# Kernel optimization log

Measured on AMD Instinct MI355X. Metric: run time of the kernel, lower is better.

## Reference

```python
import jax, jax.numpy as jnp
import numpy as np
from math import sqrt

B, H, S, D = 4, 16, 2048, 64
NEG = -1000000000.0

def setup_inputs() -> dict:
    key = jax.random.key(0)
    kq, kk, kv, km = jax.random.split(key, 4)
    Q = jax.random.normal(kq, (B, H, S, D), dtype=jnp.float32)
    K = jax.random.normal(kk, (B, H, S, D), dtype=jnp.float32)
    V = jax.random.normal(kv, (B, H, S, D), dtype=jnp.float32)
    mask = jax.random.uniform(km, (B, 1, S, S)) < 0.1
    return {"Q": Q, "K": K, "V": V, "mask": mask}

def reference(Q, K, V, mask) -> jnp.ndarray:
    # scores: [B,H,S,S]
    scores = jnp.einsum('bhqd,bhkd->bhqk', Q, K)
    scores = jnp.where(mask, NEG, scores)
    attn = jax.nn.softmax(scores / sqrt(Q.shape[-1]), axis=-1)
    return jnp.einsum('bhqk,bhkd->bhqd', attn, V)
```

## Files before the change

kernel.cpp:

```cpp
#include <hip/hip_runtime.h>


#define SEQ 2048
#define DIM 64
#define NBH 64
#define LOG2E 1.44269504088896340736f
#define SCL (0.125f * LOG2E)
#define NEG_SCALED -1.25e8f

typedef short bf16x8 __attribute__((ext_vector_type(8)));
typedef float f32x4 __attribute__((ext_vector_type(4)));
typedef float f32x16 __attribute__((ext_vector_type(16)));

static __device__ __forceinline__ unsigned short f2bf(float f) {
    unsigned int u = __float_as_uint(f);
    u += 0x7fffu + ((u >> 16) & 1u);
    return (unsigned short)(u >> 16);
}

#define GLD16(gp, lp) __builtin_amdgcn_global_load_lds( \
    (const __attribute__((address_space(1))) unsigned int*)(gp), \
    (__attribute__((address_space(3))) unsigned int*)(lp), 16, 0, 0)

__global__ __launch_bounds__(256)
void prep_all_kernel(const float* __restrict__ K, const float* __restrict__ V,
                     const int* __restrict__ M,
                     unsigned short* __restrict__ Kb, unsigned short* __restrict__ Vt,
                     unsigned int* __restrict__ Mpt) {
    const int x = blockIdx.x;
    const int t = threadIdx.x;
    if (x < 4096) {
        size_t i0 = ((size_t)x * 256 + t) * 8;
        float4 a = *(const float4*)(K + i0);
        float4 b = *(const float4*)(K + i0 + 4);
        union { uint4 u; unsigned short s[8]; } w;
        w.s[0] = f2bf(a.x); w.s[1] = f2bf(a.y); w.s[2] = f2bf(a.z); w.s[3] = f2bf(a.w);
        w.s[4] = f2bf(b.x); w.s[5] = f2bf(b.y); w.s[6] = f2bf(b.z); w.s[7] = f2bf(b.w);
        *(uint4*)(Kb + i0) = w.u;
    } else if (x < 6144) {
        __shared__ __align__(16) unsigned short T[64 * 64];
        const int vb = x - 4096;
        const int bh = vb >> 5;
        const int k0 = (vb & 31) * 64;
        {
            const float* Vb = V + ((size_t)bh * SEQ + k0) * DIM;
            #pragma unroll
            for (int j = 0; j < 4; ++j) {
                const int fi = (j * 256 + t) * 4;
                const int kk = fi >> 6;
                const int d0 = fi & 63;
                float4 f = *(const float4*)(Vb + fi);
                const int u  = (kk & ~12) | ((kk & 4) << 1) | ((kk & 8) >> 1);
                const int cs = (d0 >> 4) ^ ((u >> 3) & 3);
                union { uint2 q; unsigned short s[4]; } w4;
                w4.s[0] = f2bf(f.x); w4.s[1] = f2bf(f.y);
                w4.s[2] = f2bf(f.z); w4.s[3] = f2bf(f.w);
                *(uint2*)&T[u * 64 + cs * 16 + (d0 & 15)] = w4.q;
            }
        }
        __syncthreads();
        {
            const int kc = t & 7;
            const int dp = t >> 3;
            const int ch = (dp >> 3) ^ (kc & 3);
            const unsigned int* T32 = (const unsigned int*)T;
            union { uint4 u; unsigned short s[8]; } o0, o1;
            #pragma unroll
            for (int i = 0; i < 8; ++i) {
                unsigned int v = T32[(8 * kc + i) * 32 + ch * 8 + (dp & 7)];
                o0.s[i] = (unsigned short)v;
                o1.s[i] = (unsigned short)(v >> 16);
            }
            unsigned short* op = Vt + ((size_t)bh * DIM + 2 * dp) * SEQ + k0 + 8 * kc;
            *(uint4*)op         = o0.u;
            *(uint4*)(op + SEQ) = o1.u;
        }
    } else {
        __shared__ unsigned int Wt[64][8];
        const int m  = x - 6144;
        const int b  = m >> 8;
        const int q0 = ((m >> 3) & 31) * 64;
        const int k0 = (m & 7) * 256;
        const int w  = t >> 6, l = t & 63;
        #pragma unroll 4
        for (int row = 0; row < 16; ++row) {
            const int q = q0 + w * 16 + row;
            int4 v4 = *(const int4*)(M + ((size_t)b * SEQ + q) * SEQ + k0 + l * 4);
            unsigned int nib = (unsigned int)(v4.x != 0) | ((unsigned int)(v4.y != 0) << 1)
                             | ((unsigned int)(v4.z != 0) << 2) | ((unsigned int)(v4.w != 0) << 3);
            unsigned int v = nib << (4 * (l & 7));
            v |= __shfl_xor(v, 1);
            v |= __shfl_xor(v, 2);
            v |= __shfl_xor(v, 4);
            if ((l & 7) == 0) Wt[w * 16 + row][l >> 3] = v;
        }
        __syncthreads();
        {
            const int q = t & 63, g0 = t >> 6;
            #pragma unroll
            for (int gg = 0; gg < 2; ++gg) {
                const int g = g0 + gg * 4;
                Mpt[((size_t)b * 64 + (k0 >> 5) + g) * SEQ + q0 + q] = Wt[q][g];
            }
        }
    }
}

__global__ __launch_bounds__(256, 4)
void attn_main_kernel(const float* __restrict__ Q,
                      const unsigned short* __restrict__ Kb,
                      const unsigned short* __restrict__ Vt,
                      const unsigned int* __restrict__ Mpt,
                      float* __restrict__ O)
{
    const int n    = blockIdx.y * gridDim.x + blockIdx.x;
    const int bh   = ((n & 7) << 3) | (n >> 7);
    const int q0   = ((n >> 3) & 15) * 128;
    const int b    = bh >> 4;
    const int tid  = threadIdx.x;
    const int wave = tid >> 6;
    const int lane = tid & 63;
    const int h    = lane >> 5;
    const int q32  = lane & 31;
    const int sh4  = 4 * h;

    __shared__ __align__(16) unsigned short Kt[2][32 * 64];
    __shared__ __align__(16) unsigned short Vs[2][64 * 32];

    const unsigned short* Kbh = Kb + (size_t)bh * SEQ * DIM;
    const unsigned short* Vbh = Vt + (size_t)bh * SEQ * DIM;

    bf16x8 qf[4];
    {
        const float* qp = Q + ((size_t)bh * SEQ + q0 + wave * 32 + q32) * DIM + h * 8;
        #pragma unroll
        for (int dc = 0; dc < 4; ++dc) {
            float4 xx = *(const float4*)(qp + dc * 16);
            float4 yy = *(const float4*)(qp + dc * 16 + 4);
            qf[dc][0] = (short)f2bf(xx.x * SCL); qf[dc][1] = (short)f2bf(xx.y * SCL);
            qf[dc][2] = (short)f2bf(xx.z * SCL); qf[dc][3] = (short)f2bf(xx.w * SCL);
            qf[dc][4] = (short)f2bf(yy.x * SCL); qf[dc][5] = (short)f2bf(yy.y * SCL);
            qf[dc][6] = (short)f2bf(yy.z * SCL); qf[dc][7] = (short)f2bf(yy.w * SCL);
        }
    }

    const int kkey  = wave * 8 + (lane >> 3);
    const int kclog = (lane & 7) ^ (lane >> 3);
    const unsigned short* kg = Kbh + (size_t)kkey * DIM + kclog * 8;
    const int vd    = wave * 16 + (lane >> 2);
    const int vclog = (lane & 3) ^ ((lane >> 3) & 3);
    const unsigned short* vg = Vbh + (size_t)vd * SEQ + vclog * 8;
    unsigned short* kl[2] = { &Kt[0][wave * 512], &Kt[1][wave * 512] };
    unsigned short* vl[2] = { &Vs[0][wave * 512], &Vs[1][wave * 512] };

    const unsigned int* mp = Mpt + (size_t)b * 64 * SEQ + (q0 + wave * 32 + q32);

    f32x16 acc[2];
    #pragma unroll
    for (int i = 0; i < 16; ++i) { acc[0][i] = 0.f; acc[1][i] = 0.f; }
    float ls0 = 0.f, ls1 = 0.f, ls2 = 0.f, ls3 = 0.f;

    GLD16(kg, kl[0]);
    GLD16(vg, vl[0]);
    unsigned int mw = mp[0];

    #pragma unroll 2
    for (int it = 0; it < SEQ / 32; ++it) {
        __syncthreads();

        unsigned int mw_n = 0;
        if (it + 1 < SEQ / 32) {
            const unsigned short* kgn = kg + (size_t)(it + 1) * 32 * DIM;
            const unsigned short* vgn = vg + (size_t)(it + 1) * 32;
            int nb = (it + 1) & 1;
            GLD16(kgn, kl[nb]);
            GLD16(vgn, vl[nb]);
            mw_n = mp[(it + 1) * SEQ];
        }

        const unsigned short* Ktb = Kt[it & 1];
        const unsigned short* Vsb = Vs[it & 1];

        const unsigned int mq = mw >> sh4;
        f32x16 sc;
        #pragma unroll
        for (int r = 0; r < 16; ++r) {
            const int s = (r & 3) + 8 * (r >> 2);
            sc[r] = __int_as_float(__builtin_amdgcn_sbfe(mq, s, 1) & 0xC2C80000u);
        }

        __builtin_amdgcn_s_setprio(1);
        #pragma unroll
        for (int dc = 0; dc < 4; ++dc) {
            const int pos = (dc * 2 + h) ^ (q32 & 7);
            bf16x8 kf = *(const bf16x8*)(Ktb + q32 * 64 + pos * 8);
            sc = __builtin_amdgcn_mfma_f32_32x32x16_bf16(kf, qf[dc], sc, 0, 0, 0);
        }
        __builtin_amdgcn_s_setprio(0);

        float pv[16];
        #pragma unroll
        for (int r = 0; r < 16; ++r) pv[r] = __builtin_amdgcn_exp2f(sc[r]);

        #pragma unroll
        for (int r = 0; r < 16; r += 4) {
            ls0 += pv[r + 0];
            ls1 += pv[r + 1];
            ls2 += pv[r + 2];
            ls3 += pv[r + 3];
        }

        unsigned int pk[8];
        #pragma unroll
        for (int m = 0; m < 8; ++m) {
            asm("v_cvt_pk_bf16_f32 %0, %1, %2"
                : "=v"(pk[m]) : "v"(pv[2 * m]), "v"(pv[2 * m + 1]));
        }

        __builtin_amdgcn_s_setprio(1);
        #pragma unroll
        for (int kk = 0; kk < 2; ++kk) {
            union { unsigned int u[4]; bf16x8 v; } fr;
            fr.u[0] = pk[4 * kk + 0];
            fr.u[1] = pk[4 * kk + 1];
            fr.u[2] = pk[4 * kk + 2];
            fr.u[3] = pk[4 * kk + 3];
            #pragma unroll
            for (int dh = 0; dh < 2; ++dh) {
                const int d   = dh * 32 + q32;
                const int pos = (kk * 2 + h) ^ ((q32 >> 1) & 3);
                bf16x8 vf = *(const bf16x8*)(Vsb + d * 32 + pos * 8);
                acc[dh] = __builtin_amdgcn_mfma_f32_32x32x16_bf16(vf, fr.v, acc[dh], 0, 0, 0);
            }
        }
        __builtin_amdgcn_s_setprio(0);

        mw = mw_n;
    }

    float lsum = (ls0 + ls1) + (ls2 + ls3);
    lsum += __shfl_xor(lsum, 32);
    const float inv = 1.f / lsum;
    float* orow = O + ((size_t)bh * SEQ + q0 + wave * 32 + q32) * DIM;
    #pragma unroll
    for (int dh = 0; dh < 2; ++dh) {
        #pragma unroll
        for (int r23 = 0; r23 < 4; ++r23) {
            float4 w;
            w.x = acc[dh][4 * r23 + 0] * inv;
            w.y = acc[dh][4 * r23 + 1] * inv;
            w.z = acc[dh][4 * r23 + 2] * inv;
            w.w = acc[dh][4 * r23 + 3] * inv;
            *(float4*)(orow + dh * 32 + r23 * 8 + h * 4) = w;
        }
    }
}

__global__ __launch_bounds__(256)
void attn_fallback_kernel(const float* __restrict__ Q,
                          const float* __restrict__ K,
                          const float* __restrict__ V,
                          const int* __restrict__ mask,
                          float* __restrict__ O)
{
    const int bh   = blockIdx.y;
    const int b    = bh >> 4;
    const int q0   = blockIdx.x * 64;
    const int tid  = threadIdx.x;
    const int wave = tid >> 6;
    const int lane = tid & 63;
    const int quad = lane >> 4;
    const int l16  = lane & 15;

    __shared__ __align__(16) unsigned short Klds[32][72];
    __shared__ __align__(16) unsigned short VT[64][40];
    __shared__ __align__(16) unsigned short Plds[4][16][40];

    const float* Qb = Q + (size_t)bh * SEQ * DIM;
    const float* Kb = K + (size_t)bh * SEQ * DIM;
    const float* Vb = V + (size_t)bh * SEQ * DIM;
    const int*   Mb = mask + (size_t)b * SEQ * SEQ;

    const int qrow_frag = q0 + wave * 16 + l16;
    bf16x8 qf0, qf1;
    {
        const float* qp = Qb + (size_t)qrow_frag * DIM + quad * 8;
        #pragma unroll
        for (int i = 0; i < 8; ++i) {
            qf0[i] = (short)f2bf(qp[i]);
            qf1[i] = (short)f2bf(qp[32 + i]);
        }
    }

    f32x4 acc[4];
    #pragma unroll
    for (int dg = 0; dg < 4; ++dg) acc[dg] = (f32x4){0.f, 0.f, 0.f, 0.f};
    float mrowv[4] = {-INFINITY, -INFINITY, -INFINITY, -INFINITY};
    float lrow[4] = {0.f, 0.f, 0.f, 0.f};

    const int skey = tid >> 3;
    const int sd0  = (tid & 7) * 8;
    const int vkey = tid & 31;
    const int vd0  = (tid >> 5) * 8;
    const int qrow_m = q0 + wave * 16 + quad * 4;

    for (int kb = 0; kb < SEQ; kb += 32) {
        __syncthreads();
        {
            const float* kp = Kb + (size_t)(kb + skey) * DIM + sd0;
            union { uint4 u4; unsigned short s[8]; } kw;
            #pragma unroll
            for (int i = 0; i < 8; ++i) kw.s[i] = f2bf(kp[i]);
            *(uint4*)&Klds[skey][sd0] = kw.u4;
        }
        {
            const float* vp = Vb + (size_t)(kb + vkey) * DIM + vd0;
            #pragma unroll
            for (int i = 0; i < 8; ++i) VT[vd0 + i][vkey] = f2bf(vp[i]);
        }
        __syncthreads();

        f32x4 scr[2];
        scr[0] = (f32x4){0.f, 0.f, 0.f, 0.f};
        scr[1] = (f32x4){0.f, 0.f, 0.f, 0.f};
        #pragma unroll
        for (int nt = 0; nt < 2; ++nt) {
            bf16x8 kf0 = *(const bf16x8*)&Klds[nt * 16 + l16][quad * 8];
            bf16x8 kf1 = *(const bf16x8*)&Klds[nt * 16 + l16][32 + quad * 8];
            scr[nt] = __builtin_amdgcn_mfma_f32_16x16x32_bf16(qf0, kf0, scr[nt], 0, 0, 0);
            scr[nt] = __builtin_amdgcn_mfma_f32_16x16x32_bf16(qf1, kf1, scr[nt], 0, 0, 0);
        }

        float x[2][4];
        #pragma unroll
        for (int nt = 0; nt < 2; ++nt)
            #pragma unroll
            for (int r = 0; r < 4; ++r) {
                int mv = Mb[(size_t)(qrow_m + r) * SEQ + kb + nt * 16 + l16];
                x[nt][r] = mv ? NEG_SCALED : scr[nt][r] * 0.125f;
            }

        float p[2][4];
        #pragma unroll
        for (int r = 0; r < 4; ++r) {
            float rm = fmaxf(x[0][r], x[1][r]);
            #pragma unroll
            for (int off = 1; off < 16; off <<= 1)
                rm = fmaxf(rm, __shfl_xor(rm, off, 16));
            float mn = fmaxf(mrowv[r], rm);
            float alpha = exp2f((mrowv[r] - mn) * LOG2E);
            mrowv[r] = mn;
            float p0 = exp2f((x[0][r] - mn) * LOG2E);
            float p1 = exp2f((x[1][r] - mn) * LOG2E);
            p[0][r] = p0; p[1][r] = p1;
            float rs = p0 + p1;
            #pragma unroll
            for (int off = 1; off < 16; off <<= 1)
                rs += __shfl_xor(rs, off, 16);
            lrow[r] = lrow[r] * alpha + rs;
            #pragma unroll
            for (int dg = 0; dg < 4; ++dg)
                acc[dg][r] *= alpha;
        }

        #pragma unroll
        for (int nt = 0; nt < 2; ++nt)
            #pragma unroll
            for (int r = 0; r < 4; ++r)
                Plds[wave][quad * 4 + r][nt * 16 + l16] = f2bf(p[nt][r]);

        bf16x8 pf = *(const bf16x8*)&Plds[wave][l16][quad * 8];

        #pragma unroll
        for (int dg = 0; dg < 4; ++dg) {
            bf16x8 vf = *(const bf16x8*)&VT[dg * 16 + l16][quad * 8];
            acc[dg] = __builtin_amdgcn_mfma_f32_16x16x32_bf16(pf, vf, acc[dg], 0, 0, 0);
        }
    }

    float* Ob = O + (size_t)bh * SEQ * DIM;
    #pragma unroll
    for (int r = 0; r < 4; ++r) {
        float inv = 1.f / lrow[r];
        #pragma unroll
        for (int dg = 0; dg < 4; ++dg)
            Ob[(size_t)(qrow_m + r) * DIM + dg * 16 + l16] = acc[dg][r] * inv;
    }
}

extern "C" void kernel_launch(void* const* d_in, const int* in_sizes, int n_in,
                              void* d_out, int out_size, void* d_ws, size_t ws_size,
                              hipStream_t stream) {
    const float* Q = (const float*)d_in[0];
    const float* K = (const float*)d_in[1];
    const float* V = (const float*)d_in[2];
    const int* mask = (const int*)d_in[3];
    float*        O = (float*)d_out;

    const size_t szK = (size_t)NBH * SEQ * DIM * 2;
    const size_t szV = (size_t)NBH * SEQ * DIM * 2;
    const size_t szM = (size_t)4 * SEQ * (SEQ / 32) * 4;
    const size_t need = szK + szV + szM;

    if (ws_size >= need) {
        unsigned short* Kb = (unsigned short*)d_ws;
        unsigned short* Vt = (unsigned short*)((char*)d_ws + szK);
        unsigned int*  Mpt = (unsigned int*)((char*)d_ws + szK + szV);

        prep_all_kernel<<<dim3(7168), 256, 0, stream>>>(K, V, mask, Kb, Vt, Mpt);
        attn_main_kernel<<<dim3(SEQ / 128, NBH), 256, 0, stream>>>(Q, Kb, Vt, Mpt, O);
    } else {
        attn_fallback_kernel<<<dim3(SEQ / 64, NBH), 256, 0, stream>>>(Q, K, V, mask, O);
    }
}
```

Baseline: 270.6 us.

## Process two 32-key tiles per barrier and reorder prep kernel blocks

The main attention loop now loads and processes 64 keys per iteration as two 32-key sub-tiles. Both QK^T MFMAs run before either softmax/PV stage, so the exp work of one tile can overlap with the matrix ops of the other. This halves the number of __syncthreads barriers and doubles the shared memory for K/V buffers, which may reduce occupancy and raise register pressure. The prep kernel also reorders its block ranges so the mask-packing blocks run first.

```diff
diff --git a/kernel.cpp b/kernel.cpp
--- a/kernel.cpp
+++ b/kernel.cpp
@@ -29,55 +29,9 @@
                      unsigned int* __restrict__ Mpt) {
     const int x = blockIdx.x;
     const int t = threadIdx.x;
-    if (x < 4096) {
-        size_t i0 = ((size_t)x * 256 + t) * 8;
-        float4 a = *(const float4*)(K + i0);
-        float4 b = *(const float4*)(K + i0 + 4);
-        union { uint4 u; unsigned short s[8]; } w;
-        w.s[0] = f2bf(a.x); w.s[1] = f2bf(a.y); w.s[2] = f2bf(a.z); w.s[3] = f2bf(a.w);
-        w.s[4] = f2bf(b.x); w.s[5] = f2bf(b.y); w.s[6] = f2bf(b.z); w.s[7] = f2bf(b.w);
-        *(uint4*)(Kb + i0) = w.u;
-    } else if (x < 6144) {
-        __shared__ __align__(16) unsigned short T[64 * 64];
-        const int vb = x - 4096;
-        const int bh = vb >> 5;
-        const int k0 = (vb & 31) * 64;
-        {
-            const float* Vb = V + ((size_t)bh * SEQ + k0) * DIM;
-            #pragma unroll
-            for (int j = 0; j < 4; ++j) {
-                const int fi = (j * 256 + t) * 4;
-                const int kk = fi >> 6;
-                const int d0 = fi & 63;
-                float4 f = *(const float4*)(Vb + fi);
-                const int u  = (kk & ~12) | ((kk & 4) << 1) | ((kk & 8) >> 1);
-                const int cs = (d0 >> 4) ^ ((u >> 3) & 3);
-                union { uint2 q; unsigned short s[4]; } w4;
-                w4.s[0] = f2bf(f.x); w4.s[1] = f2bf(f.y);
-                w4.s[2] = f2bf(f.z); w4.s[3] = f2bf(f.w);
-                *(uint2*)&T[u * 64 + cs * 16 + (d0 & 15)] = w4.q;
-            }
-        }
-        __syncthreads();
-        {
-            const int kc = t & 7;
-            const int dp = t >> 3;
-            const int ch = (dp >> 3) ^ (kc & 3);
-            const unsigned int* T32 = (const unsigned int*)T;
-            union { uint4 u; unsigned short s[8]; } o0, o1;
-            #pragma unroll
-            for (int i = 0; i < 8; ++i) {
-                unsigned int v = T32[(8 * kc + i) * 32 + ch * 8 + (dp & 7)];
-                o0.s[i] = (unsigned short)v;
-                o1.s[i] = (unsigned short)(v >> 16);
-            }
-            unsigned short* op = Vt + ((size_t)bh * DIM + 2 * dp) * SEQ + k0 + 8 * kc;
-            *(uint4*)op         = o0.u;
-            *(uint4*)(op + SEQ) = o1.u;
-        }
-    } else {
+    if (x < 1024) {
         __shared__ unsigned int Wt[64][8];
-        const int m  = x - 6144;
+        const int m  = x;
         const int b  = m >> 8;
         const int q0 = ((m >> 3) & 31) * 64;
         const int k0 = (m & 7) * 256;
@@ -103,8 +57,104 @@
                 Mpt[((size_t)b * 64 + (k0 >> 5) + g) * SEQ + q0 + q] = Wt[q][g];
             }
         }
+    } else if (x < 5120) {
+        size_t i0 = ((size_t)(x - 1024) * 256 + t) * 8;
+        float4 a = *(const float4*)(K + i0);
+        float4 b = *(const float4*)(K + i0 + 4);
+        union { uint4 u; unsigned short s[8]; } w;
+        w.s[0] = f2bf(a.x); w.s[1] = f2bf(a.y); w.s[2] = f2bf(a.z); w.s[3] = f2bf(a.w);
+        w.s[4] = f2bf(b.x); w.s[5] = f2bf(b.y); w.s[6] = f2bf(b.z); w.s[7] = f2bf(b.w);
+        *(uint4*)(Kb + i0) = w.u;
+    } else {
+        __shared__ __align__(16) unsigned short T[64 * 64];
+        const int vb = x - 5120;
+        const int bh = vb >> 5;
+        const int k0 = (vb & 31) * 64;
+        {
+            const float* Vb = V + ((size_t)bh * SEQ + k0) * DIM;
+            #pragma unroll
+            for (int j = 0; j < 4; ++j) {
+                const int fi = (j * 256 + t) * 4;
+                const int kk = fi >> 6;
+                const int d0 = fi & 63;
+                float4 f = *(const float4*)(Vb + fi);
+                const int u  = (kk & ~12) | ((kk & 4) << 1) | ((kk & 8) >> 1);
+                const int cs = (d0 >> 4) ^ ((u >> 3) & 3);
+                union { uint2 q; unsigned short s[4]; } w4;
+                w4.s[0] = f2bf(f.x); w4.s[1] = f2bf(f.y);
+                w4.s[2] = f2bf(f.z); w4.s[3] = f2bf(f.w);
+                *(uint2*)&T[u * 64 + cs * 16 + (d0 & 15)] = w4.q;
+            }
+        }
+        __syncthreads();
+        {
+            const int kc = t & 7;
+            const int dp = t >> 3;
+            const int ch = (dp >> 3) ^ (kc & 3);
+            const unsigned int* T32 = (const unsigned int*)T;
+            union { uint4 u; unsigned short s[8]; } o0, o1;
+            #pragma unroll
+            for (int i = 0; i < 8; ++i) {
+                unsigned int v = T32[(8 * kc + i) * 32 + ch * 8 + (dp & 7)];
+                o0.s[i] = (unsigned short)v;
+                o1.s[i] = (unsigned short)(v >> 16);
+            }
+            unsigned short* op = Vt + ((size_t)bh * DIM + 2 * dp) * SEQ + k0 + 8 * kc;
+            *(uint4*)op         = o0.u;
+            *(uint4*)(op + SEQ) = o1.u;
+        }
     }
 }
+
+
+#define TILE_QK(sc, Ktb, mqv)                                                   \
+    {                                                                           \
+        _Pragma("unroll")                                                       \
+        for (int r = 0; r < 16; ++r) {                                          \
+            const int s_ = (r & 3) + 8 * (r >> 2);                              \
+            sc[r] = __int_as_float(__builtin_amdgcn_sbfe(mqv, s_, 1) & 0xC2C80000u); \
+        }                                                                       \
+        __builtin_amdgcn_s_setprio(1);                                          \
+        _Pragma("unroll")                                                       \
+        for (int dc = 0; dc < 4; ++dc) {                                        \
+            const int pos = (dc * 2 + h) ^ (q32 & 7);                           \
+            bf16x8 kf = *(const bf16x8*)((Ktb) + q32 * 64 + pos * 8);           \
+            sc = __builtin_amdgcn_mfma_f32_32x32x16_bf16(kf, qf[dc], sc, 0, 0, 0); \
+        }                                                                       \
+        __builtin_amdgcn_s_setprio(0);                                          \
+    }
+
+#define TILE_SMPV(sc, Vsb)                                                      \
+    {                                                                           \
+        float pv_[16];                                                          \
+        _Pragma("unroll")                                                       \
+        for (int r = 0; r < 16; ++r) pv_[r] = __builtin_amdgcn_exp2f(sc[r]);    \
+        _Pragma("unroll")                                                       \
+        for (int r = 0; r < 16; r += 4) {                                       \
+            ls0 += pv_[r + 0]; ls1 += pv_[r + 1];                               \
+            ls2 += pv_[r + 2]; ls3 += pv_[r + 3];                               \
+        }                                                                       \
+        unsigned int pk_[8];                                                    \
+        _Pragma("unroll")                                                       \
+        for (int m = 0; m < 8; ++m)                                             \
+            asm("v_cvt_pk_bf16_f32 %0, %1, %2"                                  \
+                : "=v"(pk_[m]) : "v"(pv_[2 * m]), "v"(pv_[2 * m + 1]));         \
+        __builtin_amdgcn_s_setprio(1);                                          \
+        _Pragma("unroll")                                                       \
+        for (int kk = 0; kk < 2; ++kk) {                                        \
+            union { unsigned int u[4]; bf16x8 v; } fr;                          \
+            fr.u[0] = pk_[4 * kk + 0]; fr.u[1] = pk_[4 * kk + 1];               \
+            fr.u[2] = pk_[4 * kk + 2]; fr.u[3] = pk_[4 * kk + 3];               \
+            _Pragma("unroll")                                                   \
+            for (int dh = 0; dh < 2; ++dh) {                                    \
+                const int d = dh * 32 + q32;                                    \
+                const int pos = (kk * 2 + h) ^ ((q32 >> 1) & 3);                \
+                bf16x8 vf = *(const bf16x8*)((Vsb) + d * 32 + pos * 8);         \
+                acc[dh] = __builtin_amdgcn_mfma_f32_32x32x16_bf16(vf, fr.v, acc[dh], 0, 0, 0); \
+            }                                                                   \
+        }                                                                       \
+        __builtin_amdgcn_s_setprio(0);                                          \
+    }
 
 __global__ __launch_bounds__(256, 4)
 void attn_main_kernel(const float* __restrict__ Q,
@@ -124,8 +174,8 @@
     const int q32  = lane & 31;
     const int sh4  = 4 * h;
 
-    __shared__ __align__(16) unsigned short Kt[2][32 * 64];
-    __shared__ __align__(16) unsigned short Vs[2][64 * 32];
+    __shared__ __align__(16) unsigned short Kt[2][2][32 * 64];
+    __shared__ __align__(16) unsigned short Vs[2][2][64 * 32];
 
     const unsigned short* Kbh = Kb + (size_t)bh * SEQ * DIM;
     const unsigned short* Vbh = Vt + (size_t)bh * SEQ * DIM;
@@ -150,8 +200,8 @@
     const int vd    = wave * 16 + (lane >> 2);
     const int vclog = (lane & 3) ^ ((lane >> 3) & 3);
     const unsigned short* vg = Vbh + (size_t)vd * SEQ + vclog * 8;
-    unsigned short* kl[2] = { &Kt[0][wave * 512], &Kt[1][wave * 512] };
-    unsigned short* vl[2] = { &Vs[0][wave * 512], &Vs[1][wave * 512] };
+    unsigned short* kl0 = &Kt[0][0][wave * 512];
+    unsigned short* vl0 = &Vs[0][0][wave * 512];
 
     const unsigned int* mp = Mpt + (size_t)b * 64 * SEQ + (q0 + wave * 32 + q32);
 
@@ -160,82 +210,45 @@
     for (int i = 0; i < 16; ++i) { acc[0][i] = 0.f; acc[1][i] = 0.f; }
     float ls0 = 0.f, ls1 = 0.f, ls2 = 0.f, ls3 = 0.f;
 
-    GLD16(kg, kl[0]);
-    GLD16(vg, vl[0]);
-    unsigned int mw = mp[0];
+    GLD16(kg,                     kl0);
+    GLD16(kg + (size_t)32 * DIM,  kl0 + 2048);
+    GLD16(vg,                     vl0);
+    GLD16(vg + 32,                vl0 + 2048);
+    unsigned int mw0 = mp[0];
+    unsigned int mw1 = mp[SEQ];
 
     #pragma unroll 2
-    for (int it = 0; it < SEQ / 32; ++it) {
+    for (int g = 0; g < SEQ / 64; ++g) {
         __syncthreads();
 
-        unsigned int mw_n = 0;
-        if (it + 1 < SEQ / 32) {
-            const unsigned short* kgn = kg + (size_t)(it + 1) * 32 * DIM;
-            const unsigned short* vgn = vg + (size_t)(it + 1) * 32;
-            int nb = (it + 1) & 1;
-            GLD16(kgn, kl[nb]);
-            GLD16(vgn, vl[nb]);
-            mw_n = mp[(it + 1) * SEQ];
-        }
-
-        const unsigned short* Ktb = Kt[it & 1];
-        const unsigned short* Vsb = Vs[it & 1];
-
-        const unsigned int mq = mw >> sh4;
-        f32x16 sc;
-        #pragma unroll
-        for (int r = 0; r < 16; ++r) {
-            const int s = (r & 3) + 8 * (r >> 2);
-            sc[r] = __int_as_float(__builtin_amdgcn_sbfe(mq, s, 1) & 0xC2C80000u);
-        }
-
-        __builtin_amdgcn_s_setprio(1);
-        #pragma unroll
-        for (int dc = 0; dc < 4; ++dc) {
-            const int pos = (dc * 2 + h) ^ (q32 & 7);
-            bf16x8 kf = *(const bf16x8*)(Ktb + q32 * 64 + pos * 8);
-            sc = __builtin_amdgcn_mfma_f32_32x32x16_bf16(kf, qf[dc], sc, 0, 0, 0);
-        }
-        __builtin_amdgcn_s_setprio(0);
-
-        float pv[16];
-        #pragma unroll
-        for (int r = 0; r < 16; ++r) pv[r] = __builtin_amdgcn_exp2f(sc[r]);
-
-        #pragma unroll
-        for (int r = 0; r < 16; r += 4) {
-            ls0 += pv[r + 0];
-            ls1 += pv[r + 1];
-            ls2 += pv[r + 2];
-            ls3 += pv[r + 3];
-        }
-
-        unsigned int pk[8];
-        #pragma unroll
-        for (int m = 0; m < 8; ++m) {
-            asm("v_cvt_pk_bf16_f32 %0, %1, %2"
-                : "=v"(pk[m]) : "v"(pv[2 * m]), "v"(pv[2 * m + 1]));
-        }
-
-        __builtin_amdgcn_s_setprio(1);
-        #pragma unroll
-        for (int kk = 0; kk < 2; ++kk) {
-            union { unsigned int u[4]; bf16x8 v; } fr;
-            fr.u[0] = pk[4 * kk + 0];
-            fr.u[1] = pk[4 * kk + 1];
-            fr.u[2] = pk[4 * kk + 2];
-            fr.u[3] = pk[4 * kk + 3];
-            #pragma unroll
-            for (int dh = 0; dh < 2; ++dh) {
-                const int d   = dh * 32 + q32;
-                const int pos = (kk * 2 + h) ^ ((q32 >> 1) & 3);
-                bf16x8 vf = *(const bf16x8*)(Vsb + d * 32 + pos * 8);
-                acc[dh] = __builtin_amdgcn_mfma_f32_32x32x16_bf16(vf, fr.v, acc[dh], 0, 0, 0);
-            }
-        }
-        __builtin_amdgcn_s_setprio(0);
-
-        mw = mw_n;
+        unsigned int mwn0 = 0, mwn1 = 0;
+        if (g + 1 < SEQ / 64) {
+            const size_t ko = (size_t)(g + 1) * 64 * DIM;
+            const size_t vo = (size_t)(g + 1) * 64;
+            const int nb = (g + 1) & 1;
+            GLD16(kg + ko,                 kl0 + nb * 4096);
+            GLD16(kg + ko + 32 * DIM,      kl0 + nb * 4096 + 2048);
+            GLD16(vg + vo,                 vl0 + nb * 4096);
+            GLD16(vg + vo + 32,            vl0 + nb * 4096 + 2048);
+            mwn0 = mp[(2 * g + 2) * SEQ];
+            mwn1 = mp[(2 * g + 3) * SEQ];
+        }
+
+        const int cb = g & 1;
+        const unsigned short* Kt0 = &Kt[cb][0][0];
+        const unsigned short* Kt1 = &Kt[cb][1][0];
+        const unsigned short* Vs0 = &Vs[cb][0][0];
+        const unsigned short* Vs1 = &Vs[cb][1][0];
+        const unsigned int mq0 = mw0 >> sh4;
+        const unsigned int mq1 = mw1 >> sh4;
+
+        f32x16 sc0, sc1;
+        TILE_QK(sc0, Kt0, mq0);
+        TILE_QK(sc1, Kt1, mq1);
+        TILE_SMPV(sc0, Vs0);
+        TILE_SMPV(sc1, Vs1);
+
+        mw0 = mwn0; mw1 = mwn1;
     }
 
     float lsum = (ls0 + ls1) + (ls2 + ls3);
```

Measured after the change: 271.4 us. Within noise of the previous version (+0.3%).
